# Performance work log

Hardware: AMD Instinct MI355X
Metric: run time of the kernel (lower is better)

Reference implementation:

```python
import jax, jax.numpy as jnp
import numpy as np

B, T, V, D, H, HS, FF, L = 4, 1024, 32000, 1024, 16, 64, 4096, 8
STD = 0.02

def _ln(x, g, b, eps=1e-5):
    m = x.mean(-1, keepdims=True)
    v = ((x - m) ** 2).mean(-1, keepdims=True)
    return (x - m) / jnp.sqrt(v + eps) * g + b

def setup_inputs() -> dict:
    key = jax.random.key(0)
    ks = jax.random.split(key, 16)
    n = lambda k, shp: jax.random.normal(k, shp, dtype=jnp.float32) * STD
    inp = {
        "idx": jax.random.randint(ks[0], (B, T), 0, V),
        "tok_emb": n(ks[1], (V, D)),
        "pos_emb": n(ks[2], (T, D)),
        # per-layer stacked attention weights; [D, H, HS] per layer (no bias)
        "Wq": n(ks[3], (L, D, H, HS)),
        "Wk": n(ks[4], (L, D, H, HS)),
        "Wv": n(ks[5], (L, D, H, HS)),
        "Wp": n(ks[6], (L, H * HS, D)),
        "bp": jnp.zeros((L, D), jnp.float32),
        "ln1_g": jnp.ones((L, D), jnp.float32),
        "ln1_b": jnp.zeros((L, D), jnp.float32),
        "ln2_g": jnp.ones((L, D), jnp.float32),
        "ln2_b": jnp.zeros((L, D), jnp.float32),
        "W1": n(ks[7], (L, D, FF)),
        "b1": jnp.zeros((L, FF), jnp.float32),
        "W2": n(ks[8], (L, FF, D)),
        "b2": jnp.zeros((L, D), jnp.float32),
        "lnf_g": jnp.ones((D,), jnp.float32),
        "lnf_b": jnp.zeros((D,), jnp.float32),
        "Wlm": n(ks[9], (D, V)),
        "blm": jnp.zeros((V,), jnp.float32),
    }
    return inp

def reference(idx, tok_emb, pos_emb, Wq, Wk, Wv, Wp, bp, ln1_g, ln1_b,
              ln2_g, ln2_b, W1, b1, W2, b2, lnf_g, lnf_b, Wlm, blm):
    Bb, Tt = idx.shape
    x = tok_emb[idx] + pos_emb[:Tt]                      # [B,T,D]
    causal = jnp.tril(jnp.ones((Tt, Tt), bool))          # tril mask
    for l in range(L):
        xn = _ln(x, ln1_g[l], ln1_b[l])
        q = jnp.einsum('btd,dhk->bhtk', xn, Wq[l])
        k = jnp.einsum('btd,dhk->bhtk', xn, Wk[l])
        v = jnp.einsum('btd,dhk->bhtk', xn, Wv[l])
        w = jnp.einsum('bhtk,bhsk->bhts', q, k) * (HS ** -0.5)
        w = jnp.where(causal, w, -jnp.inf)
        w = jax.nn.softmax(w, axis=-1)
        o = jnp.einsum('bhts,bhsk->bhtk', w, v)
        o = o.transpose(0, 2, 1, 3).reshape(Bb, Tt, H * HS)  # concat heads
        x = x + o @ Wp[l] + bp[l]
        xn = _ln(x, ln2_g[l], ln2_b[l])
        x = x + jax.nn.relu(xn @ W1[l] + b1[l]) @ W2[l] + b2[l]
    x = _ln(x, lnf_g, lnf_b)
    logits = x @ Wlm + blm                               # [B,T,V]
    return logits
```

## Files before the change

kernel.cpp:

```cpp
#include <hip/hip_runtime.h>
#include <cstdint>

typedef __attribute__((ext_vector_type(4))) float f32x4;
typedef __attribute__((ext_vector_type(8))) short s16x8;
typedef __attribute__((ext_vector_type(4))) short s16x4;
typedef unsigned short u16;
typedef unsigned int u32;
typedef __attribute__((address_space(1))) void gas_void;
typedef __attribute__((address_space(3))) void las_void;

#define B_ 4
#define T_ 1024
#define V_ 32000
#define D_ 1024
#define H_ 16
#define HS_ 64
#define FF_ 4096
#define L_ 8
#define BT_ (B_ * T_)

__device__ __forceinline__ float bf2f(u16 h) { return __uint_as_float(((u32)h) << 16); }
__device__ __forceinline__ u16 f2bf(float f) {
  u32 u = __float_as_uint(f);
  u += 0x7fffu + ((u >> 16) & 1u);
  return (u16)(u >> 16);
}

__device__ __forceinline__ void gld16(const void* g, void* l) {
  __builtin_amdgcn_global_load_lds((gas_void*)(uintptr_t)g,
                                   (las_void*)(u32)(uintptr_t)l, 16, 0, 0);
}


template <int EPI>
__global__ __launch_bounds__(256) void gemm_bt(
    const u16* __restrict__ A, const u16* __restrict__ Bt,
    const float* __restrict__ bias, float* Cf, u16* Cb,
    int M, int N, int K) {
  __shared__ u16 lds[2][2][4096];
  const int tid = threadIdx.x;
  const int lane = tid & 63;
  const int lr = lane & 15, hi = lane >> 4;
  const int wid = tid >> 6;
  const int wm = wid >> 1, wn = wid & 1;
  const int row0 = blockIdx.y << 7, col0 = blockIdx.x << 7;
  const int NT = K >> 5;
  const int wbase = (tid & ~63) << 4;
  const int xo = ((hi + (lr >> 1)) & 3) << 4;

  f32x4 acc[4][4];
#pragma unroll
  for (int i = 0; i < 4; ++i)
#pragma unroll
    for (int j = 0; j < 4; ++j) acc[i][j] = f32x4{0.f, 0.f, 0.f, 0.f};

  auto stage = [&](int buf, int kt) {
#pragma unroll
    for (int c = 0; c < 2; ++c) {
      const int o = (c << 12) + (tid << 4);
      const int r = o >> 6;
      const int ko = ((((o >> 4) & 3) - (r >> 1)) & 3) << 3;
      gld16(A + (size_t)(row0 + r) * K + (kt << 5) + ko,
            (char*)&lds[buf][0][0] + (c << 12) + wbase);
      gld16(Bt + (size_t)(col0 + r) * K + (kt << 5) + ko,
            (char*)&lds[buf][1][0] + (c << 12) + wbase);
    }
  };

  stage(0, 0);
  __syncthreads();
  int cur = 0;
  for (int kt = 0; kt < NT; ++kt) {
    if (kt + 1 < NT) stage(cur ^ 1, kt + 1);
    const char* As = (const char*)&lds[cur][0][0];
    const char* Bs = (const char*)&lds[cur][1][0];
    s16x8 af[4], bfr[4];
#pragma unroll
    for (int i = 0; i < 4; ++i) {
      const int ra = (wm << 6) + (i << 4) + lr;
      af[i] = *(const s16x8*)(As + (ra << 6) + xo);
      const int rb = (wn << 6) + (i << 4) + lr;
      bfr[i] = *(const s16x8*)(Bs + (rb << 6) + xo);
    }
#pragma unroll
    for (int i = 0; i < 4; ++i)
#pragma unroll
      for (int j = 0; j < 4; ++j)
        acc[i][j] =
            __builtin_amdgcn_mfma_f32_16x16x32_bf16(af[i], bfr[j], acc[i][j], 0, 0, 0);
    __syncthreads();
    cur ^= 1;
  }

  const int gr = row0 + (wm << 6);
  const int gc = col0 + (wn << 6);
#pragma unroll
  for (int j = 0; j < 4; ++j) {
    const int col = gc + (j << 4) + lr;
    const float bv = (EPI != 0) ? bias[col] : 0.f;
#pragma unroll
    for (int i = 0; i < 4; ++i) {
#pragma unroll
      for (int rg = 0; rg < 4; ++rg) {
        const int row = gr + (i << 4) + (hi << 2) + rg;
        const size_t off = (size_t)row * N + col;
        float val = acc[i][j][rg] + bv;
        if constexpr (EPI == 1) val += Cf[off];
        if constexpr (EPI == 2) val = fmaxf(val, 0.f);
        if constexpr (EPI == 0 || EPI == 2) Cb[off] = f2bf(val);
        else Cf[off] = val;
      }
    }
  }
}

template <int EPI>
__global__ __launch_bounds__(256) void gemm_bt64(
    const u16* __restrict__ A, const u16* __restrict__ Bt,
    const float* __restrict__ bias, float* Cf, u16* Cb,
    int M, int N, int K) {
  __shared__ u16 lds[2][6144];
  const int tid = threadIdx.x;
  const int lane = tid & 63;
  const int lr = lane & 15, hi = lane >> 4;
  const int w = tid >> 6;
  const int row0 = blockIdx.y << 6, col0 = blockIdx.x << 7;
  const int NT = K >> 5;
  const int wbase = (tid & ~63) << 4;
  const int schunk = tid & 3;
  const int xo = ((hi + (lr >> 1)) & 3) << 4;

  f32x4 acc[4][2];
#pragma unroll
  for (int i = 0; i < 4; ++i)
#pragma unroll
    for (int j = 0; j < 2; ++j) acc[i][j] = f32x4{0.f, 0.f, 0.f, 0.f};

  auto stage = [&](int buf, int kt) {
    const int r = tid >> 2;
    {
      const int ko = ((schunk - (r >> 1)) & 3) << 3;
      gld16(A + (size_t)(row0 + r) * K + (kt << 5) + ko,
            (char*)&lds[buf][0] + wbase);
    }
#pragma unroll
    for (int sh = 0; sh < 2; ++sh) {
      const int rb = (sh << 6) + r;
      const int ko = ((schunk - (rb >> 1)) & 3) << 3;
      gld16(Bt + (size_t)(col0 + rb) * K + (kt << 5) + ko,
            (char*)&lds[buf][2048] + (sh << 12) + wbase);
    }
  };

  stage(0, 0);
  __syncthreads();
  int cur = 0;
  for (int kt = 0; kt < NT; ++kt) {
    if (kt + 1 < NT) stage(cur ^ 1, kt + 1);
    const char* As = (const char*)&lds[cur][0];
    const char* Bs = (const char*)&lds[cur][2048];
    s16x8 af[4], bf2[2];
#pragma unroll
    for (int i = 0; i < 4; ++i)
      af[i] = *(const s16x8*)(As + (((i << 4) + lr) << 6) + xo);
#pragma unroll
    for (int j = 0; j < 2; ++j)
      bf2[j] = *(const s16x8*)(Bs + (((w << 5) + (j << 4) + lr) << 6) + xo);
#pragma unroll
    for (int i = 0; i < 4; ++i)
#pragma unroll
      for (int j = 0; j < 2; ++j)
        acc[i][j] =
            __builtin_amdgcn_mfma_f32_16x16x32_bf16(af[i], bf2[j], acc[i][j], 0, 0, 0);
    __syncthreads();
    cur ^= 1;
  }

  const int gc = col0 + (w << 5);
#pragma unroll
  for (int j = 0; j < 2; ++j) {
    const int col = gc + (j << 4) + lr;
    const float bv = (EPI != 0) ? bias[col] : 0.f;
#pragma unroll
    for (int i = 0; i < 4; ++i) {
#pragma unroll
      for (int rg = 0; rg < 4; ++rg) {
        const int row = row0 + (i << 4) + (hi << 2) + rg;
        const size_t off = (size_t)row * N + col;
        float val = acc[i][j][rg] + bv;
        if constexpr (EPI == 1) val += Cf[off];
        if constexpr (EPI == 2) val = fmaxf(val, 0.f);
        if constexpr (EPI == 0 || EPI == 2) Cb[off] = f2bf(val);
        else Cf[off] = val;
      }
    }
  }
}

__global__ __launch_bounds__(256) void ln_kernel(const float* __restrict__ x,
                                                 const float* __restrict__ gw,
                                                 const float* __restrict__ bw,
                                                 u16* __restrict__ out) {
  const int lane = threadIdx.x & 63;
  const size_t r = ((size_t)blockIdx.x << 2) + (threadIdx.x >> 6);
  const float* xp = x + (r << 10);
  f32x4 v[4];
  float s = 0.f, q = 0.f;
#pragma unroll
  for (int j = 0; j < 4; ++j) {
    v[j] = *(const f32x4*)(xp + (lane << 2) + (j << 8));
#pragma unroll
    for (int e = 0; e < 4; ++e) {
      s += v[j][e];
      q += v[j][e] * v[j][e];
    }
  }
#pragma unroll
  for (int off = 32; off; off >>= 1) {
    s += __shfl_xor(s, off);
    q += __shfl_xor(q, off);
  }
  const float mean = s * (1.f / 1024.f);
  const float var = q * (1.f / 1024.f) - mean * mean;
  const float rstd = rsqrtf(var + 1e-5f);
  u16* op = out + (r << 10);
#pragma unroll
  for (int j = 0; j < 4; ++j) {
    const f32x4 g4 = *(const f32x4*)(gw + (lane << 2) + (j << 8));
    const f32x4 b4 = *(const f32x4*)(bw + (lane << 2) + (j << 8));
    s16x4 o4;
#pragma unroll
    for (int e = 0; e < 4; ++e)
      o4[e] = (short)f2bf((v[j][e] - mean) * rstd * g4[e] + b4[e]);
    *(s16x4*)(op + (lane << 2) + (j << 8)) = o4;
  }
}

__global__ __launch_bounds__(256) void embed_kernel(const int* __restrict__ idx,
                                                    const float* __restrict__ tok,
                                                    const float* __restrict__ pos,
                                                    float* __restrict__ x) {
  const int r = blockIdx.x, tid = threadIdx.x;
  const int t = r & (T_ - 1);
  const int tk = idx[r];
  f32x4 a = *(const f32x4*)(tok + ((size_t)tk << 10) + (tid << 2));
  f32x4 p = *(const f32x4*)(pos + ((size_t)t << 10) + (tid << 2));
  *(f32x4*)(x + ((size_t)r << 10) + (tid << 2)) = a + p;
}

#define TCONV_BODY(SRC, DST, KK, NN)                                           \
  {                                                                            \
    __shared__ float tile[32][33];                                             \
    const int tx = threadIdx.x & 31, ty = threadIdx.x >> 5;                    \
    const int n0 = blockIdx.x << 5, k0 = blockIdx.y << 5;                      \
    _Pragma("unroll")                                                          \
    for (int i = 0; i < 32; i += 8)                                            \
      tile[ty + i][tx] = (SRC)[(size_t)(k0 + ty + i) * (NN) + n0 + tx];        \
    __syncthreads();                                                           \
    _Pragma("unroll")                                                          \
    for (int i = 0; i < 32; i += 8)                                            \
      (DST)[(size_t)(n0 + ty + i) * (KK) + k0 + tx] = f2bf(tile[tx][ty + i]);  \
  }

__global__ __launch_bounds__(256) void tconv_qkvp(
    const float* __restrict__ Wq, const float* __restrict__ Wk,
    const float* __restrict__ Wv, const float* __restrict__ Wp,
    u16* __restrict__ WqkvT, u16* __restrict__ WpT) {
  const int z = blockIdx.z;
  const int l = z >> 2, m = z & 3;
  const float* src;
  u16* dst;
  if (m == 0) { src = Wq + (size_t)l * D_ * D_; dst = WqkvT + (size_t)l * 3072 * D_; }
  else if (m == 1) { src = Wk + (size_t)l * D_ * D_; dst = WqkvT + (size_t)l * 3072 * D_ + D_ * D_; }
  else if (m == 2) { src = Wv + (size_t)l * D_ * D_; dst = WqkvT + (size_t)l * 3072 * D_ + 2 * D_ * D_; }
  else { src = Wp + (size_t)l * D_ * D_; dst = WpT + (size_t)l * D_ * D_; }
  TCONV_BODY(src, dst, D_, D_)
}

__global__ __launch_bounds__(256) void tconv_w1(const float* __restrict__ W1,
                                                u16* __restrict__ W1T) {
  const int l = blockIdx.z;
  TCONV_BODY(W1 + (size_t)l * D_ * FF_, W1T + (size_t)l * FF_ * D_, D_, FF_)
}

__global__ __launch_bounds__(256) void tconv_w2(const float* __restrict__ W2,
                                                u16* __restrict__ W2T) {
  const int l = blockIdx.z;
  TCONV_BODY(W2 + (size_t)l * FF_ * D_, W2T + (size_t)l * D_ * FF_, FF_, D_)
}

__global__ __launch_bounds__(256) void tconv_kernel(const float* __restrict__ src,
                                                    u16* __restrict__ dst, int K, int N) {
  TCONV_BODY(src, dst, K, N)
}

__global__ __launch_bounds__(512, 4) void fattn_kernel(const u16* __restrict__ qkv,
                                                       u16* __restrict__ o) {
  const int flat = (int)blockIdx.x;
  const int xcd = flat & 7, seq = flat >> 3;
  const int pair = (xcd << 3) + (seq >> 3);
  const int qt = seq & 7;
  const int h = pair & 15, b = pair >> 4;
  const int tid = threadIdx.x;
  const int lane = tid & 63;
  const int lr = lane & 15, hi = lane >> 4;
  const int w = tid >> 6;
  __shared__ alignas(16) u16 Kl[2][4096];
  __shared__ alignas(16) u16 Vt[2][4096];

  const size_t bT = (size_t)(b * T_);
  const int q_row = (qt << 7) + (w << 4) + lr;
  const int qtw = (qt << 1) + (w >> 2);
  const size_t qbase = (bT + q_row) * 3072 + (h << 6);
  s16x8 aq[2];
  aq[0] = *(const s16x8*)(qkv + qbase + hi * 8);
  aq[1] = *(const s16x8*)(qkv + qbase + 32 + hi * 8);

  f32x4 ofr[4];
#pragma unroll
  for (int j = 0; j < 4; ++j) ofr[j] = f32x4{0.f, 0.f, 0.f, 0.f};
  float mrun = -1e30f, lsum = 0.f;
  const float SCL = 0.125f * 1.44269504f;

  uint4 vr0;

#define STAGEK(BUF, KT)                                                        \
  {                                                                            \
    const int r_ = tid >> 3;                                                   \
    const int il_ = (((tid & 7) << 4)) ^ ((r_ & 7) << 4);                      \
    gld16(qkv + (bT + ((KT) << 6) + r_) * 3072 + 1024 + (h << 6) + (il_ >> 1), \
          (char*)&Kl[BUF][0] + ((tid & 448) << 4));                            \
  }
#define LOADV(KT)                                                              \
  {                                                                            \
    vr0 = *(const uint4*)(qkv + (bT + ((KT) << 6) + lane) * 3072 + 2048 +      \
                          (h << 6) + (w << 3));                                \
  }
#define WRITEV(BUF)                                                            \
  {                                                                            \
    const u16* p0_ = (const u16*)&vr0;                                         \
    _Pragma("unroll")                                                          \
    for (int j_ = 0; j_ < 8; ++j_)                                             \
      Vt[BUF][(((w << 3) + j_) << 6) + (lane ^ (j_ << 3))] = p0_[j_];          \
  }

  STAGEK(0, 0)
  LOADV(0)
  asm volatile("s_waitcnt vmcnt(0)" ::: "memory");
  WRITEV(0)
  asm volatile("s_waitcnt lgkmcnt(0)" ::: "memory");
  __builtin_amdgcn_sched_barrier(0);
  __builtin_amdgcn_s_barrier();

  const int nkt = (qt << 1) + 2;
  int cur = 0;
  for (int kt = 0; kt < nkt; ++kt) {
    if (kt + 1 < nkt) {
      STAGEK(cur ^ 1, kt + 1)
      LOADV(kt + 1)
    }

    const bool full = (kt > qtw);
    f32x4 s[4];
    if (!full) {
#pragma unroll
      for (int j = 0; j < 4; ++j) s[j] = f32x4{0.f, 0.f, 0.f, 0.f};
      __builtin_amdgcn_s_setprio(1);
#pragma unroll
      for (int kk = 0; kk < 2; ++kk)
#pragma unroll
        for (int j = 0; j < 4; ++j) {
          const int rb = (j << 4) + lr;
          const s16x8 bk = *(const s16x8*)((const char*)&Kl[cur][0] + (rb << 7) +
                                           ((((kk << 2) + hi) ^ (rb & 7)) << 4));
          s[j] = __builtin_amdgcn_mfma_f32_16x16x32_bf16(bk, aq[kk], s[j], 0, 0, 0);
        }
      __builtin_amdgcn_s_setprio(0);
      if (kt == qtw) {
        const int qr = q_row & 63;
#pragma unroll
        for (int j = 0; j < 4; ++j)
#pragma unroll
          for (int rg = 0; rg < 4; ++rg) {
            const int kvr = (j << 4) + (hi << 2) + rg;
            s[j][rg] = (kvr > qr) ? -1e30f : s[j][rg] * SCL;
          }
      } else {
#pragma unroll
        for (int j = 0; j < 4; ++j) s[j] = s[j] * SCL;
      }
    } else {
#pragma unroll
      for (int j = 0; j < 4; ++j) s[j] = f32x4{-1e30f, -1e30f, -1e30f, -1e30f};
    }

    float mx = fmaxf(fmaxf(s[0][0], s[0][1]), fmaxf(s[0][2], s[0][3]));
#pragma unroll
    for (int j = 1; j < 4; ++j)
#pragma unroll
      for (int rg = 0; rg < 4; ++rg) mx = fmaxf(mx, s[j][rg]);
    mx = fmaxf(mx, __shfl_xor(mx, 16));
    mx = fmaxf(mx, __shfl_xor(mx, 32));
    const float mn = fmaxf(mrun, mx);
    const float sc = exp2f(mrun - mn);
    mrun = mn;
    float rs = 0.f;
#pragma unroll
    for (int j = 0; j < 4; ++j)
#pragma unroll
      for (int rg = 0; rg < 4; ++rg) {
        const float e = exp2f(s[j][rg] - mn);
        s[j][rg] = e;
        rs += e;
      }
    rs += __shfl_xor(rs, 16);
    rs += __shfl_xor(rs, 32);
    lsum = lsum * sc + rs;
    float scO[4];
#pragma unroll
    for (int rg = 0; rg < 4; ++rg) scO[rg] = __shfl(sc, (hi << 2) + rg);
#pragma unroll
    for (int j2 = 0; j2 < 4; ++j2)
#pragma unroll
      for (int rg = 0; rg < 4; ++rg) ofr[j2][rg] *= scO[rg];

    if (!full) {
      s16x8 pb[2];
#pragma unroll
      for (int kk = 0; kk < 2; ++kk)
#pragma unroll
        for (int i = 0; i < 4; ++i) {
          pb[kk][i] = (short)f2bf(s[2 * kk][i]);
          pb[kk][4 + i] = (short)f2bf(s[2 * kk + 1][i]);
        }

      __builtin_amdgcn_s_setprio(1);
#pragma unroll
      for (int kk = 0; kk < 2; ++kk)
#pragma unroll
        for (int j2 = 0; j2 < 4; ++j2) {
          const int drow = (j2 << 4) + lr;
          const int swz = (drow & 7) << 3;
          const int base = drow << 6;
          const s16x4 lo = *(const s16x4*)&Vt[cur][base + (((kk << 5) + (hi << 2)) ^ swz)];
          const s16x4 hv = *(const s16x4*)&Vt[cur][base + (((kk << 5) + 16 + (hi << 2)) ^ swz)];
          const s16x8 vb = __builtin_shufflevector(lo, hv, 0, 1, 2, 3, 4, 5, 6, 7);
          ofr[j2] = __builtin_amdgcn_mfma_f32_16x16x32_bf16(pb[kk], vb, ofr[j2], 0, 0, 0);
        }
      __builtin_amdgcn_s_setprio(0);
    }

    if (kt + 1 < nkt) {
      asm volatile("s_waitcnt vmcnt(0)" ::: "memory");
      WRITEV(cur ^ 1)
    }
    asm volatile("s_waitcnt lgkmcnt(0)" ::: "memory");
    __builtin_amdgcn_sched_barrier(0);
    __builtin_amdgcn_s_barrier();
    cur ^= 1;
  }

  const float rinv = 1.f / lsum;
  float rO[4];
#pragma unroll
  for (int rg = 0; rg < 4; ++rg) rO[rg] = __shfl(rinv, (hi << 2) + rg);
#pragma unroll
  for (int j2 = 0; j2 < 4; ++j2)
#pragma unroll
    for (int rg = 0; rg < 4; ++rg) {
      const int row = (qt << 7) + (w << 4) + (hi << 2) + rg;
      const int col = (h << 6) + (j2 << 4) + lr;
      o[(bT + row) * 1024 + col] = f2bf(ofr[j2][rg] * rO[rg]);
    }
#undef STAGEK
#undef LOADV
#undef WRITEV
}

extern "C" void kernel_launch(void* const* d_in, const int* in_sizes, int n_in,
                              void* d_out, int out_size, void* d_ws, size_t ws_size,
                              hipStream_t stream) {
  (void)in_sizes; (void)n_in; (void)out_size; (void)ws_size;
  const int* idx = (const int*)d_in[0];
  const float* tokE = (const float*)d_in[1];
  const float* posE = (const float*)d_in[2];
  const float* Wq = (const float*)d_in[3];
  const float* Wk = (const float*)d_in[4];
  const float* Wv = (const float*)d_in[5];
  const float* Wp = (const float*)d_in[6];
  const float* bp = (const float*)d_in[7];
  const float* ln1g = (const float*)d_in[8];
  const float* ln1b = (const float*)d_in[9];
  const float* ln2g = (const float*)d_in[10];
  const float* ln2b = (const float*)d_in[11];
  const float* W1 = (const float*)d_in[12];
  const float* b1 = (const float*)d_in[13];
  const float* W2 = (const float*)d_in[14];
  const float* b2 = (const float*)d_in[15];
  const float* lnfg = (const float*)d_in[16];
  const float* lnfb = (const float*)d_in[17];
  const float* Wlm = (const float*)d_in[18];
  const float* blm = (const float*)d_in[19];

  char* p = (char*)d_ws;
  float* x = (float*)p;   p += (size_t)BT_ * D_ * 4;
  u16* xn = (u16*)p;      p += (size_t)BT_ * D_ * 2;
  u16* qkv = (u16*)p;     p += (size_t)BT_ * 3072 * 2;
  u16* ob = (u16*)p;      p += (size_t)BT_ * D_ * 2;
  u16* hb = (u16*)p;      p += (size_t)BT_ * FF_ * 2;
  u16* WqkvT = (u16*)p;   p += (size_t)L_ * 3072 * D_ * 2;
  u16* WpT = (u16*)p;     p += (size_t)L_ * D_ * D_ * 2;
  u16* W1T = (u16*)p;     p += (size_t)L_ * FF_ * D_ * 2;
  u16* W2T = (u16*)p;     p += (size_t)L_ * D_ * FF_ * 2;
  u16* WlmT = (u16*)p;    p += (size_t)V_ * D_ * 2;

  dim3 blk(256);
  dim3 blk512(512);
  tconv_qkvp<<<dim3(32, 32, 32), blk, 0, stream>>>(Wq, Wk, Wv, Wp, WqkvT, WpT);
  tconv_w1<<<dim3(128, 32, 8), blk, 0, stream>>>(W1, W1T);
  tconv_w2<<<dim3(32, 128, 8), blk, 0, stream>>>(W2, W2T);
  tconv_kernel<<<dim3(1000, 32), blk, 0, stream>>>(Wlm, WlmT, D_, V_);

  embed_kernel<<<dim3(BT_), blk, 0, stream>>>(idx, tokE, posE, x);

  for (int l = 0; l < L_; ++l) {
    ln_kernel<<<dim3(BT_ / 4), blk, 0, stream>>>(x, ln1g + l * D_, ln1b + l * D_, xn);
    gemm_bt<0><<<dim3(24, 32), blk, 0, stream>>>(xn, WqkvT + (size_t)l * 3072 * D_,
                                                 nullptr, nullptr, qkv, BT_, 3072, D_);
    fattn_kernel<<<dim3(512), blk512, 0, stream>>>(qkv, ob);
    gemm_bt64<1><<<dim3(8, 64), blk, 0, stream>>>(ob, WpT + (size_t)l * D_ * D_,
                                                  bp + l * D_, x, nullptr, BT_, D_, D_);
    ln_kernel<<<dim3(BT_ / 4), blk, 0, stream>>>(x, ln2g + l * D_, ln2b + l * D_, xn);
    gemm_bt<2><<<dim3(32, 32), blk, 0, stream>>>(xn, W1T + (size_t)l * FF_ * D_,
                                                 b1 + l * FF_, nullptr, hb, BT_, FF_, D_);
    gemm_bt64<1><<<dim3(8, 64), blk, 0, stream>>>(hb, W2T + (size_t)l * D_ * FF_,
                                                  b2 + l * D_, x, nullptr, BT_, D_, FF_);
  }
  ln_kernel<<<dim3(BT_ / 4), blk, 0, stream>>>(x, lnfg, lnfb, xn);
  gemm_bt<3><<<dim3(250, 32), blk, 0, stream>>>(xn, WlmT, blm, (float*)d_out, nullptr,
                                                BT_, V_, D_);
}
```

Measured before the change: 2.563 ms.

## Add swizzled LM-head GEMM kernel and vectorize weight transpose-convert kernels

Adds a dedicated LM-head GEMM that uses a 1D grid remapped by an XCD-style interleave, so neighbouring blocks share weight tiles in cache. It also replaces the 32x32 transpose/convert tile with a 64x64 tile that uses vector loads and 16-byte bf16 stores, cutting the number of memory instructions during weight preprocessing. Separately, the residual read-add is removed from the gemm_bt EPI==1 path, which appears unused by gemm_bt callers. That last edit risks changing semantics if any caller relied on it.

```diff
diff --git a/kernel.cpp b/kernel.cpp
--- a/kernel.cpp
+++ b/kernel.cpp
@@ -105,10 +105,88 @@
         const int row = gr + (i << 4) + (hi << 2) + rg;
         const size_t off = (size_t)row * N + col;
         float val = acc[i][j][rg] + bv;
-        if constexpr (EPI == 1) val += Cf[off];
         if constexpr (EPI == 2) val = fmaxf(val, 0.f);
         if constexpr (EPI == 0 || EPI == 2) Cb[off] = f2bf(val);
         else Cf[off] = val;
+      }
+    }
+  }
+}
+
+__global__ __launch_bounds__(256) void gemm_bt_lm(
+    const u16* __restrict__ A, const u16* __restrict__ Bt,
+    const float* __restrict__ bias, float* Cf,
+    int M, int N, int K) {
+  __shared__ u16 lds[2][2][4096];
+  const int tid = threadIdx.x;
+  const int lane = tid & 63;
+  const int lr = lane & 15, hi = lane >> 4;
+  const int wid = tid >> 6;
+  const int wm = wid >> 1, wn = wid & 1;
+  const int flat = (int)blockIdx.x;
+  const int logical = (flat & 7) * ((int)gridDim.x >> 3) + (flat >> 3);
+  const int row0 = (logical & 31) << 7;
+  const int col0 = (logical >> 5) << 7;
+  const int NT = K >> 5;
+  const int wbase = (tid & ~63) << 4;
+  const int xo = ((hi + (lr >> 1)) & 3) << 4;
+
+  f32x4 acc[4][4];
+#pragma unroll
+  for (int i = 0; i < 4; ++i)
+#pragma unroll
+    for (int j = 0; j < 4; ++j) acc[i][j] = f32x4{0.f, 0.f, 0.f, 0.f};
+
+  auto stage = [&](int buf, int kt) {
+#pragma unroll
+    for (int c = 0; c < 2; ++c) {
+      const int o = (c << 12) + (tid << 4);
+      const int r = o >> 6;
+      const int ko = ((((o >> 4) & 3) - (r >> 1)) & 3) << 3;
+      gld16(A + (size_t)(row0 + r) * K + (kt << 5) + ko,
+            (char*)&lds[buf][0][0] + (c << 12) + wbase);
+      gld16(Bt + (size_t)(col0 + r) * K + (kt << 5) + ko,
+            (char*)&lds[buf][1][0] + (c << 12) + wbase);
+    }
+  };
+
+  stage(0, 0);
+  __syncthreads();
+  int cur = 0;
+  for (int kt = 0; kt < NT; ++kt) {
+    if (kt + 1 < NT) stage(cur ^ 1, kt + 1);
+    const char* As = (const char*)&lds[cur][0][0];
+    const char* Bs = (const char*)&lds[cur][1][0];
+    s16x8 af[4], bfr[4];
+#pragma unroll
+    for (int i = 0; i < 4; ++i) {
+      const int ra = (wm << 6) + (i << 4) + lr;
+      af[i] = *(const s16x8*)(As + (ra << 6) + xo);
+      const int rb = (wn << 6) + (i << 4) + lr;
+      bfr[i] = *(const s16x8*)(Bs + (rb << 6) + xo);
+    }
+#pragma unroll
+    for (int i = 0; i < 4; ++i)
+#pragma unroll
+      for (int j = 0; j < 4; ++j)
+        acc[i][j] =
+            __builtin_amdgcn_mfma_f32_16x16x32_bf16(af[i], bfr[j], acc[i][j], 0, 0, 0);
+    __syncthreads();
+    cur ^= 1;
+  }
+
+  const int gr = row0 + (wm << 6);
+  const int gc = col0 + (wn << 6);
+#pragma unroll
+  for (int j = 0; j < 4; ++j) {
+    const int col = gc + (j << 4) + lr;
+    const float bv = bias[col];
+#pragma unroll
+    for (int i = 0; i < 4; ++i) {
+#pragma unroll
+      for (int rg = 0; rg < 4; ++rg) {
+        const int row = gr + (i << 4) + (hi << 2) + rg;
+        Cf[(size_t)row * N + col] = acc[i][j][rg] + bv;
       }
     }
   }
@@ -250,16 +328,26 @@
 
 #define TCONV_BODY(SRC, DST, KK, NN)                                           \
   {                                                                            \
-    __shared__ float tile[32][33];                                             \
-    const int tx = threadIdx.x & 31, ty = threadIdx.x >> 5;                    \
-    const int n0 = blockIdx.x << 5, k0 = blockIdx.y << 5;                      \
+    __shared__ float tile[64][65];                                             \
+    const int tid = threadIdx.x;                                               \
+    const int n0 = blockIdx.x << 6, k0 = blockIdx.y << 6;                      \
     _Pragma("unroll")                                                          \
-    for (int i = 0; i < 32; i += 8)                                            \
-      tile[ty + i][tx] = (SRC)[(size_t)(k0 + ty + i) * (NN) + n0 + tx];        \
+    for (int it = 0; it < 4; ++it) {                                           \
+      const int k = (tid >> 4) + (it << 4);                                    \
+      const int n = (tid & 15) << 2;                                           \
+      *(f32x4*)&tile[k][n] =                                                   \
+          *(const f32x4*)((SRC) + (size_t)(k0 + k) * (NN) + n0 + n);           \
+    }                                                                          \
     __syncthreads();                                                           \
     _Pragma("unroll")                                                          \
-    for (int i = 0; i < 32; i += 8)                                            \
-      (DST)[(size_t)(n0 + ty + i) * (KK) + k0 + tx] = f2bf(tile[tx][ty + i]);  \
+    for (int it = 0; it < 2; ++it) {                                           \
+      const int n = (tid >> 3) + (it << 5);                                    \
+      const int kp = (tid & 7) << 3;                                           \
+      s16x8 o;                                                                 \
+      _Pragma("unroll")                                                        \
+      for (int j = 0; j < 8; ++j) o[j] = (short)f2bf(tile[kp + j][n]);         \
+      *(s16x8*)((DST) + (size_t)(n0 + n) * (KK) + k0 + kp) = o;                \
+    }                                                                          \
   }
 
 __global__ __launch_bounds__(256) void tconv_qkvp(
@@ -516,10 +604,10 @@
 
   dim3 blk(256);
   dim3 blk512(512);
-  tconv_qkvp<<<dim3(32, 32, 32), blk, 0, stream>>>(Wq, Wk, Wv, Wp, WqkvT, WpT);
-  tconv_w1<<<dim3(128, 32, 8), blk, 0, stream>>>(W1, W1T);
-  tconv_w2<<<dim3(32, 128, 8), blk, 0, stream>>>(W2, W2T);
-  tconv_kernel<<<dim3(1000, 32), blk, 0, stream>>>(Wlm, WlmT, D_, V_);
+  tconv_qkvp<<<dim3(16, 16, 32), blk, 0, stream>>>(Wq, Wk, Wv, Wp, WqkvT, WpT);
+  tconv_w1<<<dim3(64, 16, 8), blk, 0, stream>>>(W1, W1T);
+  tconv_w2<<<dim3(16, 64, 8), blk, 0, stream>>>(W2, W2T);
+  tconv_kernel<<<dim3(500, 16), blk, 0, stream>>>(Wlm, WlmT, D_, V_);
 
   embed_kernel<<<dim3(BT_), blk, 0, stream>>>(idx, tokE, posE, x);
 
@@ -537,6 +625,6 @@
                                                   b2 + l * D_, x, nullptr, BT_, D_, FF_);
   }
   ln_kernel<<<dim3(BT_ / 4), blk, 0, stream>>>(x, lnfg, lnfb, xn);
-  gemm_bt<3><<<dim3(250, 32), blk, 0, stream>>>(xn, WlmT, blm, (float*)d_out, nullptr,
-                                                BT_, V_, D_);
-}
+  gemm_bt_lm<<<dim3(8000), blk, 0, stream>>>(xn, WlmT, blm, (float*)d_out,
+                                             BT_, V_, D_);
+}
```

Result: no change. 2.533 ms (-1.2%).
